# Kernel tuning notes

Hardware: AMD Instinct MI355X
Metric: run time of the kernel (lower is better)

## Reference

```python
import jax, jax.numpy as jnp
import numpy as np

N_NODES = 100000
N_EDGES = 1000000
D_FEAT = 128
N_ACTIONS = 64


def setup_inputs() -> dict:
    key = jax.random.key(0)
    ks = jax.random.split(key, 8)
    return {
        "x": jax.random.normal(ks[0], (N_NODES, D_FEAT), dtype=jnp.float32),
        "edge_index": jax.random.randint(ks[1], (2, N_EDGES), 0, N_NODES, dtype=jnp.int64),
        "W_gcn": jax.random.normal(ks[2], (D_FEAT, D_FEAT), dtype=jnp.float32) / np.sqrt(D_FEAT),
        "b_gcn": jax.random.normal(ks[3], (D_FEAT,), dtype=jnp.float32) * 0.02,
        "W_high": jax.random.normal(ks[4], (D_FEAT, N_ACTIONS), dtype=jnp.float32) / np.sqrt(D_FEAT),
        "b_high": jax.random.normal(ks[5], (N_ACTIONS,), dtype=jnp.float32) * 0.02,
        "W_low": jax.random.normal(ks[6], (D_FEAT, N_ACTIONS), dtype=jnp.float32) / np.sqrt(D_FEAT),
        "b_low": jax.random.normal(ks[7], (N_ACTIONS,), dtype=jnp.float32) * 0.02,
    }


def gcn_conv(x, edge_index, W, b):
    """PyG GCNConv: add self-loops, symmetric normalization, aggregate, linear."""
    n = x.shape[0]
    loops = jnp.arange(n, dtype=edge_index.dtype)
    src = jnp.concatenate([edge_index[0], loops])  # message sources
    dst = jnp.concatenate([edge_index[1], loops])  # message targets
    # degree of each target node (edge weight 1, incl. self-loop)
    deg = jax.ops.segment_sum(jnp.ones(src.shape[0], dtype=x.dtype), dst, num_segments=n)
    dinv = jax.lax.rsqrt(deg)  # deg >= 1 thanks to self-loops
    norm = dinv[src] * dinv[dst]  # [E+N]
    h = x @ W  # [N, D] dense transform first (cheaper than transforming messages)
    agg = jax.ops.segment_sum(h[src] * norm[:, None], dst, num_segments=n)
    return agg + b


def reference(x, edge_index, W_gcn, b_gcn, W_high, b_high, W_low, b_low):
    h = gcn_conv(x, edge_index, W_gcn, b_gcn)  # [N, D]
    high = h @ W_high + b_high  # [N, A]
    low = h @ W_low + b_low     # [N, A]
    return (high, low)
```

## Files before the change

kernel.cpp:

```cpp
#include <hip/hip_runtime.h>


#define BLOCK 256
#define SB 512
#define NB_MAX 784
#define SLOT 2048
#define CHUNK_MAX 2048
#define CONV_BLOCKS 4096

typedef _Float16 half8 __attribute__((ext_vector_type(8)));
typedef _Float16 half4 __attribute__((ext_vector_type(4)));
typedef float f32x4 __attribute__((ext_vector_type(4)));


__global__ __launch_bounds__(BLOCK) void k_prep(const float* __restrict__ x,
                                                const float* __restrict__ Wg,
                                                const float* __restrict__ Wh,
                                                const float* __restrict__ Wl,
                                                const float* __restrict__ bg,
                                                const float* __restrict__ bh,
                                                const float* __restrict__ bl,
                                                _Float16* __restrict__ WfT,
                                                float* __restrict__ bf,
                                                int* __restrict__ cursor,
                                                _Float16* __restrict__ xh,
                                                int n, int NB) {
    int b = blockIdx.x;
    if (b < 16) {
        int r = b * 8 + (threadIdx.x >> 5);
        int c0 = (threadIdx.x & 31) * 4;
        float a0 = 0.f, a1 = 0.f, a2 = 0.f, a3 = 0.f;
        for (int j = 0; j < 128; j++) {
            float wg = Wg[r * 128 + j];
            float4 wc;
            if (c0 < 64) wc = *(const float4*)(Wh + j * 64 + c0);
            else         wc = *(const float4*)(Wl + j * 64 + (c0 - 64));
            a0 += wg * wc.x; a1 += wg * wc.y; a2 += wg * wc.z; a3 += wg * wc.w;
        }
        WfT[(size_t)(c0 + 0) * 128 + r] = (_Float16)a0;
        WfT[(size_t)(c0 + 1) * 128 + r] = (_Float16)a1;
        WfT[(size_t)(c0 + 2) * 128 + r] = (_Float16)a2;
        WfT[(size_t)(c0 + 3) * 128 + r] = (_Float16)a3;
    } else if (b == 16) {
        int c = threadIdx.x;
        if (c < 128) {
            float acc = (c < 64) ? bh[c] : bl[c - 64];
            for (int j = 0; j < 128; j++) {
                float wc = (c < 64) ? Wh[j * 64 + c] : Wl[j * 64 + (c - 64)];
                acc += bg[j] * wc;
            }
            bf[c] = acc;
        }
        for (int i = threadIdx.x; i < NB; i += BLOCK) cursor[i] = i * SLOT;
    } else {
        const float4* x4 = (const float4*)x;
        half4* o4 = (half4*)xh;
        int total = n * 32;
        int i = (b - 17) * BLOCK + threadIdx.x;
        int stride = CONV_BLOCKS * BLOCK;
        for (; i < total; i += stride) {
            float4 v = x4[i];
            half4 o;
            o.x = (_Float16)v.x; o.y = (_Float16)v.y;
            o.z = (_Float16)v.z; o.w = (_Float16)v.w;
            o4[i] = o;
        }
    }
}


__global__ __launch_bounds__(BLOCK) void k_scatter(const int* __restrict__ src,
                                                   const int* __restrict__ dst, int E,
                                                   int* __restrict__ cursor,
                                                   int2* __restrict__ ebuf, int NB) {
    __shared__ int2 stash[CHUNK_MAX];
    __shared__ int hist[NB_MAX];
    __shared__ int cur[NB_MAX];
    int blk = blockIdx.x;
    int chunk = (E + SB - 1) / SB;
    int e0 = blk * chunk, e1 = min(E, e0 + chunk);
    int m = e1 - e0;

    for (int i = threadIdx.x; i < NB; i += BLOCK) hist[i] = 0;
    __syncthreads();
    for (int i = threadIdx.x; i < m; i += BLOCK) {
        int d = dst[e0 + i], s = src[e0 + i];
        stash[i] = make_int2(d, s);
        atomicAdd(&hist[d >> 7], 1);
    }
    __syncthreads();
    for (int i = threadIdx.x; i < NB; i += BLOCK) {
        int h = hist[i];
        cur[i] = h ? atomicAdd(&cursor[i], h) : 0;
    }
    __syncthreads();
    for (int i = threadIdx.x; i < m; i += BLOCK) {
        int2 p = stash[i];
        int pos = atomicAdd(&cur[p.x >> 7], 1);
        ebuf[pos] = p;
    }
}


__global__ __launch_bounds__(BLOCK) void k_node(const int2* __restrict__ ebuf,
                                                const int* __restrict__ cursor,
                                                int2* __restrict__ off2,
                                                float* __restrict__ dinv,
                                                int* __restrict__ csr,
                                                int n) {
    __shared__ int cnt[128];
    __shared__ int pre[128];
    __shared__ int cur[128];
    int bkt = blockIdx.x;
    int t = threadIdx.x;
    int node0 = bkt << 7;
    int nn = min(128, n - node0);
    int eb0 = bkt * SLOT;
    int eb1 = cursor[bkt];

    if (t < 128) cnt[t] = 0;
    __syncthreads();
    for (int e = eb0 + t; e < eb1; e += BLOCK)
        atomicAdd(&cnt[ebuf[e].x & 127], 1);
    __syncthreads();
    if (t < 128) pre[t] = cnt[t];
    __syncthreads();
    for (int ofs = 1; ofs < 128; ofs <<= 1) {
        int v = (t < 128 && t >= ofs) ? pre[t - ofs] : 0;
        __syncthreads();
        if (t < 128) pre[t] += v;
        __syncthreads();
    }
    if (t < 128) cur[t] = pre[t] - cnt[t];
    __syncthreads();
    if (t < nn) {
        off2[node0 + t] = make_int2(eb0 + cur[t], eb0 + pre[t]);
        dinv[node0 + t] = rsqrtf((float)(cnt[t] + 1));
    }
    for (int e = eb0 + t; e < eb1; e += BLOCK) {
        int2 p = ebuf[e];
        int pos = atomicAdd(&cur[p.x & 127], 1);
        csr[eb0 + pos] = p.y;
    }
}


__global__ __launch_bounds__(BLOCK) void k_gf(const int2* __restrict__ off2,
                                              const int* __restrict__ csr,
                                              const float* __restrict__ dinv,
                                              const _Float16* __restrict__ xh,
                                              const _Float16* __restrict__ WfT,
                                              const float* __restrict__ bf,
                                              float* __restrict__ out, int n) {
    __shared__ _Float16 lds[64 * 128];
    int wave = threadIdx.x >> 6;
    int lane = threadIdx.x & 63;
    int g = lane >> 4;
    int sl = lane & 15;
    int T0 = blockIdx.x * 64;
    int wrow0 = wave * 16;

    for (int p = 0; p < 4; p++) {
        int r = wrow0 + p * 4 + g;
        int d = T0 + r;
        int dc = min(d, n - 1);
        bool valid = (d < n);
        int2 oe = off2[dc];
        float dv = valid ? dinv[dc] : 0.f;
        int beg = oe.x;
        int end = valid ? oe.y : oe.x;
        half8 xv = *(const half8*)(xh + (size_t)dc * 128 + sl * 8);
        float acc[8];
#pragma unroll
        for (int k = 0; k < 8; k++) acc[k] = dv * (float)xv[k];

        int e = beg;
        for (; e + 4 <= end; e += 4) {
            int s0 = csr[e], s1 = csr[e + 1], s2 = csr[e + 2], s3 = csr[e + 3];
            float w0 = dinv[s0], w1 = dinv[s1], w2 = dinv[s2], w3 = dinv[s3];
            half8 v0 = *(const half8*)(xh + (size_t)s0 * 128 + sl * 8);
            half8 v1 = *(const half8*)(xh + (size_t)s1 * 128 + sl * 8);
            half8 v2 = *(const half8*)(xh + (size_t)s2 * 128 + sl * 8);
            half8 v3 = *(const half8*)(xh + (size_t)s3 * 128 + sl * 8);
#pragma unroll
            for (int k = 0; k < 8; k++)
                acc[k] += w0 * (float)v0[k] + w1 * (float)v1[k]
                        + w2 * (float)v2[k] + w3 * (float)v3[k];
        }
        for (; e < end; ++e) {
            int s0 = csr[e];
            float w0 = dinv[s0];
            half8 v0 = *(const half8*)(xh + (size_t)s0 * 128 + sl * 8);
#pragma unroll
            for (int k = 0; k < 8; k++) acc[k] += w0 * (float)v0[k];
        }
        half8 o;
#pragma unroll
        for (int k = 0; k < 8; k++) o[k] = (_Float16)(dv * acc[k]);
        *(half8*)(lds + (size_t)r * 128 + ((sl ^ (r & 7)) * 8)) = o;
    }

    int l15 = sl, lk = g;
    half8 a[4];
    {
        int r = wrow0 + l15;
#pragma unroll
        for (int kk = 0; kk < 4; kk++) {
            int ch = (kk * 4 + lk) ^ (l15 & 7);
            a[kk] = *(const half8*)(lds + (size_t)r * 128 + ch * 8);
        }
    }
    f32x4 acc[8];
#pragma unroll
    for (int cf = 0; cf < 8; cf++) acc[cf] = (f32x4){0.f, 0.f, 0.f, 0.f};
#pragma unroll
    for (int kk = 0; kk < 4; kk++) {
#pragma unroll
        for (int cf = 0; cf < 8; cf++) {
            half8 bfr = *(const half8*)(WfT + (size_t)(cf * 16 + l15) * 128 + kk * 32 + lk * 8);
            acc[cf] = __builtin_amdgcn_mfma_f32_16x16x32_f16(a[kk], bfr, acc[cf], 0, 0, 0);
        }
    }
#pragma unroll
    for (int cf = 0; cf < 8; cf++) {
        int c = cf * 16 + l15;
        float bv = bf[c];
        size_t cbase = (c < 64) ? (size_t)c : (size_t)n * 64 + (size_t)(c - 64);
        int r0 = T0 + wrow0 + lk * 4;
#pragma unroll
        for (int j = 0; j < 4; j++) {
            int rr = r0 + j;
            if (rr < n) out[cbase + (size_t)rr * 64] = acc[cf][j] + bv;
        }
    }
}

extern "C" void kernel_launch(void* const* d_in, const int* in_sizes, int n_in,
                              void* d_out, int out_size, void* d_ws, size_t ws_size,
                              hipStream_t stream) {
    const float* x  = (const float*)d_in[0];
    const int*   ei = (const int*)d_in[1];
    const float* Wg = (const float*)d_in[2];
    const float* bg = (const float*)d_in[3];
    const float* Wh = (const float*)d_in[4];
    const float* bh = (const float*)d_in[5];
    const float* Wl = (const float*)d_in[6];
    const float* bl = (const float*)d_in[7];
    float* out = (float*)d_out;

    int n = in_sizes[0] / 128;
    int E = in_sizes[1] / 2;
    const int* src = ei;
    const int* dst = ei + E;
    int NB = (n + 127) >> 7;

#define WS_TAKE(ptr, type, count)                                        \
    ptr = (type*)wsp;                                                    \
    wsp = (char*)(((size_t)(wsp + (size_t)(count) * sizeof(type)) + 255) \
                  & ~(size_t)255)

    char* wsp = (char*)d_ws;
    int*      cursor; WS_TAKE(cursor, int,      NB_MAX);
    int2*     ebuf;   WS_TAKE(ebuf,   int2,     (size_t)NB_MAX * SLOT);
    int2*     off2;   WS_TAKE(off2,   int2,     n);
    float*    dinv;   WS_TAKE(dinv,   float,    n);
    int*      csr;    WS_TAKE(csr,    int,      (size_t)NB_MAX * SLOT);
    _Float16* WfT;    WS_TAKE(WfT,    _Float16, 128 * 128);
    float*    bf;     WS_TAKE(bf,     float,    128);
    _Float16* xh;     WS_TAKE(xh,     _Float16, (size_t)n * 128);

    k_prep<<<17 + CONV_BLOCKS, BLOCK, 0, stream>>>(
        x, Wg, Wh, Wl, bg, bh, bl, WfT, bf, cursor, xh, n, NB);
    k_scatter<<<SB, BLOCK, 0, stream>>>(src, dst, E, cursor, ebuf, NB);
    k_node<<<NB, BLOCK, 0, stream>>>(ebuf, cursor, off2, dinv, csr, n);
    k_gf<<<(n + 63) / 64, BLOCK, 0, stream>>>(off2, csr, dinv, xh, WfT, bf, out, n);
}
```

Measured before the change: 244.7 us.

## Fold source-degree scaling into fp16 x conversion inside k_node, shuffle-broadcast CSR indices

The fp32-to-fp16 conversion of x moves from k_prep into k_node, where each row is pre-scaled by its own dinv as it is converted. This removes the per-edge dinv[src] gather in the aggregation kernel. The aggregation loop now loads 16 CSR indices cooperatively and broadcasts them with wave shuffles, with masked 4-way unrolling, instead of every lane reading csr and dinv. Risks are extra fp16 rounding from pre-scaling, and a conversion in k_node that now runs after the scatter rather than overlapping with it.

```diff
diff --git a/kernel.cpp b/kernel.cpp
--- a/kernel.cpp
+++ b/kernel.cpp
@@ -6,15 +6,13 @@
 #define NB_MAX 784
 #define SLOT 2048
 #define CHUNK_MAX 2048
-#define CONV_BLOCKS 4096
 
 typedef _Float16 half8 __attribute__((ext_vector_type(8)));
 typedef _Float16 half4 __attribute__((ext_vector_type(4)));
 typedef float f32x4 __attribute__((ext_vector_type(4)));
 
 
-__global__ __launch_bounds__(BLOCK) void k_prep(const float* __restrict__ x,
-                                                const float* __restrict__ Wg,
+__global__ __launch_bounds__(BLOCK) void k_prep(const float* __restrict__ Wg,
                                                 const float* __restrict__ Wh,
                                                 const float* __restrict__ Wl,
                                                 const float* __restrict__ bg,
@@ -23,8 +21,7 @@
                                                 _Float16* __restrict__ WfT,
                                                 float* __restrict__ bf,
                                                 int* __restrict__ cursor,
-                                                _Float16* __restrict__ xh,
-                                                int n, int NB) {
+                                                int NB) {
     int b = blockIdx.x;
     if (b < 16) {
         int r = b * 8 + (threadIdx.x >> 5);
@@ -41,7 +38,7 @@
         WfT[(size_t)(c0 + 1) * 128 + r] = (_Float16)a1;
         WfT[(size_t)(c0 + 2) * 128 + r] = (_Float16)a2;
         WfT[(size_t)(c0 + 3) * 128 + r] = (_Float16)a3;
-    } else if (b == 16) {
+    } else {
         int c = threadIdx.x;
         if (c < 128) {
             float acc = (c < 64) ? bh[c] : bl[c - 64];
@@ -52,19 +49,6 @@
             bf[c] = acc;
         }
         for (int i = threadIdx.x; i < NB; i += BLOCK) cursor[i] = i * SLOT;
-    } else {
-        const float4* x4 = (const float4*)x;
-        half4* o4 = (half4*)xh;
-        int total = n * 32;
-        int i = (b - 17) * BLOCK + threadIdx.x;
-        int stride = CONV_BLOCKS * BLOCK;
-        for (; i < total; i += stride) {
-            float4 v = x4[i];
-            half4 o;
-            o.x = (_Float16)v.x; o.y = (_Float16)v.y;
-            o.z = (_Float16)v.z; o.w = (_Float16)v.w;
-            o4[i] = o;
-        }
     }
 }
 
@@ -104,9 +88,11 @@
 
 __global__ __launch_bounds__(BLOCK) void k_node(const int2* __restrict__ ebuf,
                                                 const int* __restrict__ cursor,
+                                                const float* __restrict__ x,
                                                 int2* __restrict__ off2,
                                                 float* __restrict__ dinv,
                                                 int* __restrict__ csr,
+                                                _Float16* __restrict__ xh,
                                                 int n) {
     __shared__ int cnt[128];
     __shared__ int pre[128];
@@ -141,6 +127,17 @@
         int2 p = ebuf[e];
         int pos = atomicAdd(&cur[p.x & 127], 1);
         csr[eb0 + pos] = p.y;
+    }
+    const float4* xr = (const float4*)(x + (size_t)node0 * 128);
+    half4* xw = (half4*)(xh + (size_t)node0 * 128);
+    for (int idx = t; idx < nn * 32; idx += BLOCK) {
+        int row = idx >> 5;
+        float dvL = rsqrtf((float)(cnt[row] + 1));
+        float4 v = xr[idx];
+        half4 o;
+        o.x = (_Float16)(dvL * v.x); o.y = (_Float16)(dvL * v.y);
+        o.z = (_Float16)(dvL * v.z); o.w = (_Float16)(dvL * v.w);
+        xw[idx] = o;
     }
 }
 
@@ -159,40 +156,42 @@
     int sl = lane & 15;
     int T0 = blockIdx.x * 64;
     int wrow0 = wave * 16;
+    int lbase = g << 4;
 
     for (int p = 0; p < 4; p++) {
         int r = wrow0 + p * 4 + g;
         int d = T0 + r;
         int dc = min(d, n - 1);
-        bool valid = (d < n);
         int2 oe = off2[dc];
-        float dv = valid ? dinv[dc] : 0.f;
+        float dv = dinv[dc];
         int beg = oe.x;
-        int end = valid ? oe.y : oe.x;
-        half8 xv = *(const half8*)(xh + (size_t)dc * 128 + sl * 8);
+        int end = (d < n) ? oe.y : oe.x;
+        half8 sv = *(const half8*)(xh + (size_t)dc * 128 + sl * 8);
         float acc[8];
 #pragma unroll
-        for (int k = 0; k < 8; k++) acc[k] = dv * (float)xv[k];
-
-        int e = beg;
-        for (; e + 4 <= end; e += 4) {
-            int s0 = csr[e], s1 = csr[e + 1], s2 = csr[e + 2], s3 = csr[e + 3];
-            float w0 = dinv[s0], w1 = dinv[s1], w2 = dinv[s2], w3 = dinv[s3];
-            half8 v0 = *(const half8*)(xh + (size_t)s0 * 128 + sl * 8);
-            half8 v1 = *(const half8*)(xh + (size_t)s1 * 128 + sl * 8);
-            half8 v2 = *(const half8*)(xh + (size_t)s2 * 128 + sl * 8);
-            half8 v3 = *(const half8*)(xh + (size_t)s3 * 128 + sl * 8);
-#pragma unroll
-            for (int k = 0; k < 8; k++)
-                acc[k] += w0 * (float)v0[k] + w1 * (float)v1[k]
-                        + w2 * (float)v2[k] + w3 * (float)v3[k];
-        }
-        for (; e < end; ++e) {
-            int s0 = csr[e];
-            float w0 = dinv[s0];
-            half8 v0 = *(const half8*)(xh + (size_t)s0 * 128 + sl * 8);
-#pragma unroll
-            for (int k = 0; k < 8; k++) acc[k] += w0 * (float)v0[k];
+        for (int k = 0; k < 8; k++) acc[k] = (float)sv[k];
+
+        for (int b0 = beg; b0 < end; b0 += 16) {
+            int take = min(16, end - b0);
+            int s = 0;
+            if (sl < take) s = csr[b0 + sl];
+            for (int j = 0; j < take; j += 4) {
+                int se0 = __shfl(s, lbase + j);
+                int se1 = __shfl(s, lbase + ((j + 1) & 15));
+                int se2 = __shfl(s, lbase + ((j + 2) & 15));
+                int se3 = __shfl(s, lbase + ((j + 3) & 15));
+                float m1 = (j + 1 < take) ? 1.f : 0.f;
+                float m2 = (j + 2 < take) ? 1.f : 0.f;
+                float m3 = (j + 3 < take) ? 1.f : 0.f;
+                half8 v0 = *(const half8*)(xh + (size_t)se0 * 128 + sl * 8);
+                half8 v1 = *(const half8*)(xh + (size_t)se1 * 128 + sl * 8);
+                half8 v2 = *(const half8*)(xh + (size_t)se2 * 128 + sl * 8);
+                half8 v3 = *(const half8*)(xh + (size_t)se3 * 128 + sl * 8);
+#pragma unroll
+                for (int k = 0; k < 8; k++)
+                    acc[k] += (float)v0[k] + m1 * (float)v1[k]
+                            + m2 * (float)v2[k] + m3 * (float)v3[k];
+            }
         }
         half8 o;
 #pragma unroll
@@ -269,9 +268,8 @@
     float*    bf;     WS_TAKE(bf,     float,    128);
     _Float16* xh;     WS_TAKE(xh,     _Float16, (size_t)n * 128);
 
-    k_prep<<<17 + CONV_BLOCKS, BLOCK, 0, stream>>>(
-        x, Wg, Wh, Wl, bg, bh, bl, WfT, bf, cursor, xh, n, NB);
+    k_prep<<<17, BLOCK, 0, stream>>>(Wg, Wh, Wl, bg, bh, bl, WfT, bf, cursor, NB);
     k_scatter<<<SB, BLOCK, 0, stream>>>(src, dst, E, cursor, ebuf, NB);
-    k_node<<<NB, BLOCK, 0, stream>>>(ebuf, cursor, off2, dinv, csr, n);
+    k_node<<<NB, BLOCK, 0, stream>>>(ebuf, cursor, x, off2, dinv, csr, xh, n);
     k_gf<<<(n + 63) / 64, BLOCK, 0, stream>>>(off2, csr, dinv, xh, WfT, bf, out, n);
 }
```

Result: no change. 245.3 us (+0.3%).
